# Optimization experiments

Measured on AMD Instinct MI355X. Metric: run time of the kernel, lower is better.

The kernel has to match this reference:

```python
import jax, jax.numpy as jnp
import numpy as np

EPS = 1e-07


def _splat_one(inp, idx4, w4, n):
    # inp: [C1, N] weighted features for one batch element
    # idx4: [4, N] int32 flat target indices (clipped)
    # w4:  [4, N] bilinear weights (zeroed where out of bounds)
    out = jnp.zeros((inp.shape[0], n), dtype=inp.dtype)
    for k in range(4):
        out = out.at[:, idx4[k]].add(inp * w4[k])
    return out


def _softsplat(x, flow, metric):
    B, C, H, W = x.shape
    N = H * W
    m = jnp.exp(metric)                      # [B,1,H,W]
    inp = jnp.concatenate([x * m, m], axis=1)  # [B,C+1,H,W]

    gy, gx = jnp.meshgrid(jnp.arange(H, dtype=x.dtype),
                          jnp.arange(W, dtype=x.dtype), indexing='ij')
    tx = gx[None] + flow[:, 0]               # [B,H,W] target x
    ty = gy[None] + flow[:, 1]               # [B,H,W] target y

    x0f = jnp.floor(tx)
    y0f = jnp.floor(ty)
    x0 = x0f.astype(jnp.int32)
    y0 = y0f.astype(jnp.int32)
    x1 = x0 + 1
    y1 = y0 + 1

    fx = tx - x0f                            # frac parts
    fy = ty - y0f
    # bilinear weights for (x0,y0),(x1,y0),(x0,y1),(x1,y1)
    w = jnp.stack([(1 - fx) * (1 - fy),
                   fx * (1 - fy),
                   (1 - fx) * fy,
                   fx * fy], axis=1)          # [B,4,H,W]
    xs = jnp.stack([x0, x1, x0, x1], axis=1)  # [B,4,H,W]
    ys = jnp.stack([y0, y0, y1, y1], axis=1)

    valid = (xs >= 0) & (xs < W) & (ys >= 0) & (ys < H)
    w = jnp.where(valid, w, 0.0).reshape(B, 4, N)
    idx = (jnp.clip(ys, 0, H - 1) * W + jnp.clip(xs, 0, W - 1)).reshape(B, 4, N)

    inp_flat = inp.reshape(B, C + 1, N)
    out = jax.vmap(lambda i, ix, ww: _splat_one(i, ix, ww, N))(inp_flat, idx, w)
    out = out.reshape(B, C + 1, H, W)
    return out[:, :-1] / (out[:, -1:] + EPS)


def setup_inputs() -> dict:
    key = jax.random.key(0)
    k1, k2, k3 = jax.random.split(key, 3)
    x = jax.random.normal(k1, (8, 64, 256, 448), dtype=jnp.float32)
    flow = jax.random.normal(k2, (8, 2, 256, 448), dtype=jnp.float32)
    metric = jax.random.normal(k3, (8, 1, 256, 448), dtype=jnp.float32)
    return {"x": x, "flow": flow, "metric": metric}


def reference(x, flow, metric):
    return _softsplat(x, flow, metric)
```

## Files before the change

### kernel.cpp

```cpp
#include <hip/hip_runtime.h>

#define EPS 1e-7f

constexpr int B = 8, C = 64, H = 256, W = 448;
constexpr int N = H * W;
constexpr int P = B * N;

constexpr int TS  = 16;
constexpr int NT  = 256;
constexpr int RW  = 8;
constexpr int WIN = 32;
constexpr int NW  = WIN * WIN;
constexpr int TGS = 40;
constexpr int K   = 15;
constexpr int CHB = 8;
constexpr int NCHUNK = C / CHB;
constexpr float FMAX = 7.0f;
constexpr int TX = W / TS, TY = H / TS;
constexpr int TILES = B * TX * TY;
constexpr int NXCD = 8;

constexpr int L_TGT = 0, L_FX = 1280, L_FY = 2304, L_EM = 3328, L_PK = 4352;
constexpr int LDS_WORDS = 8192;

typedef __fp16 h2_t __attribute__((ext_vector_type(2)));
static __device__ __forceinline__ unsigned pk2(float a, float b) {
    h2_t h = __builtin_amdgcn_cvt_pkrtz(a, b);
    return __builtin_bit_cast(unsigned, h);
}
static __device__ __forceinline__ float2 up2(unsigned u) {
    h2_t h = __builtin_bit_cast(h2_t, u);
    return make_float2((float)h.x, (float)h.y);
}

__device__ int g_flag;

__global__ void zero_flag_k() { g_flag = 0; }

__global__ __launch_bounds__(256) void flag_scan(const float* __restrict__ flow)
{
    int t = blockIdx.x * blockDim.x + threadIdx.x;
    if (t >= P) return;
    int b = t / N, p = t - b * N;
    float fdx = flow[(size_t)(b * 2 + 0) * N + p];
    float fdy = flow[(size_t)(b * 2 + 1) * N + p];
    if (fabsf(fdx) > FMAX || fabsf(fdy) > FMAX) atomicAdd(&g_flag, 1);
}

#define STAGE_LOAD(dst, gg)                                                   \
    {                                                                         \
        const int cbase = (gg) * CHB;                                         \
        const int row = tid >> 3;                                             \
        const int sc0 = (tid & 7) * 4;                                        \
        const int sh = ty0 - RW + row;                                        \
        const int sc = tx0 - RW + sc0;                                        \
        const bool v = (sh >= 0) & (sh < H) & (sc >= 0) & (sc < W);           \
        const float* bp = xb + (sh * W + sc);                                 \
        _Pragma("unroll")                                                     \
        for (int ch = 0; ch < CHB; ++ch)                                      \
            dst[ch] = v ? *(const float4*)(bp + (size_t)(cbase + ch) * N)     \
                        : make_float4(0.f, 0.f, 0.f, 0.f);                    \
    }

#define STAGE_WRITE(src, bufsel)                                              \
    {                                                                         \
        char* base = (char*)lds + (bufsel) * 16384;                           \
        _Pragma("unroll")                                                     \
        for (int k = 0; k < 4; ++k) {                                         \
            const unsigned pos = 4u * (unsigned)tid + (unsigned)k;            \
            const unsigned blk = pos ^ ((pos >> 3) & 7u);                     \
            uint4 wv;                                                         \
            wv.x = pk2(((const float*)&src[0])[k], ((const float*)&src[1])[k]); \
            wv.y = pk2(((const float*)&src[2])[k], ((const float*)&src[3])[k]); \
            wv.z = pk2(((const float*)&src[4])[k], ((const float*)&src[5])[k]); \
            wv.w = pk2(((const float*)&src[6])[k], ((const float*)&src[7])[k]); \
            *(uint4*)(base + blk * 16) = wv;                                  \
        }                                                                     \
    }

#define COMPUTE_STORE(bufsel, gg)                                             \
    {                                                                         \
        const char* bc = (const char*)lds + (bufsel) * 16384;                 \
        float a0 = 0.f, a1 = 0.f, a2 = 0.f, a3 = 0.f;                         \
        float a4 = 0.f, a5 = 0.f, a6 = 0.f, a7 = 0.f;                         \
        _Pragma("unroll")                                                     \
        for (int j = 0; j < K; ++j) {                                         \
            if (j >= kwave) break;                   \
            const uint4 v = *(const uint4*)(bc + rsp[j]);                     \
            const float wj = rw_[j];                                          \
            float2 pp;                                                        \
            pp = up2(v.x); a0 = fmaf(wj, pp.x, a0); a1 = fmaf(wj, pp.y, a1);  \
            pp = up2(v.y); a2 = fmaf(wj, pp.x, a2); a3 = fmaf(wj, pp.y, a3);  \
            pp = up2(v.z); a4 = fmaf(wj, pp.x, a4); a5 = fmaf(wj, pp.y, a5);  \
            pp = up2(v.w); a6 = fmaf(wj, pp.x, a6); a7 = fmaf(wj, pp.y, a7);  \
        }                                                                     \
        if (!ovf) {                                                           \
            ob[(size_t)((gg) * CHB + 0) * N] = a0;                            \
            ob[(size_t)((gg) * CHB + 1) * N] = a1;                            \
            ob[(size_t)((gg) * CHB + 2) * N] = a2;                            \
            ob[(size_t)((gg) * CHB + 3) * N] = a3;                            \
            ob[(size_t)((gg) * CHB + 4) * N] = a4;                            \
            ob[(size_t)((gg) * CHB + 5) * N] = a5;                            \
            ob[(size_t)((gg) * CHB + 6) * N] = a6;                            \
            ob[(size_t)((gg) * CHB + 7) * N] = a7;                            \
        }                                                                     \
    }

__global__ __launch_bounds__(NT) void softsplat_fused(
    const float* __restrict__ x,
    const float* __restrict__ flow,
    const float* __restrict__ metric,
    float* __restrict__ out,
    float* __restrict__ den)
{
    __shared__ float lds[LDS_WORDS];
    unsigned* s_tgt = (unsigned*)(lds + L_TGT);
    float*    s_fx  = lds + L_FX;
    float*    s_fy  = lds + L_FY;
    float*    s_em  = lds + L_EM;
    unsigned* s_pk  = (unsigned*)(lds + L_PK);

    int bid = blockIdx.x;
    bid = (bid % NXCD) * (TILES / NXCD) + bid / NXCD;

    const int b   = bid / (TX * TY);
    const int tp  = bid % (TX * TY);
    const int ty0 = (tp / TX) * TS;
    const int tx0 = (tp % TX) * TS;
    const int tid = threadIdx.x;

    const float* fxg = flow + (size_t)(b * 2 + 0) * N;
    const float* fyg = flow + (size_t)(b * 2 + 1) * N;
    const float* mg  = metric + (size_t)b * N;

    float mxx = 0.f, mxy = 0.f;
    for (int i = tid; i < NW; i += NT) {
        const int wy = i >> 5, wx = i & 31;
        const int sh = ty0 - RW + wy, sw = tx0 - RW + wx;
        unsigned t = 0xFFFFFFFFu;
        if (sh >= 0 && sh < H && sw >= 0 && sw < W) {
            const int sp = sh * W + sw;
            const float a = fxg[sp], bb = fyg[sp];
            if (fabsf(a) <= FMAX && fabsf(bb) <= FMAX) {
                const float xf = floorf(a), yf = floorf(bb);
                const int tx0g = sw + (int)xf + 16;
                const int ty0g = sh + (int)yf + 16;
                t = ((unsigned)ty0g << 16) | (unsigned)tx0g;
                s_fx[i] = a - xf;
                s_fy[i] = bb - yf;
                s_em[i] = __expf(mg[sp]);
                mxx = fmaxf(mxx, fabsf(a));
                mxy = fmaxf(mxy, fabsf(bb));
            }
        }
        s_tgt[wy * TGS + wx] = t;
    }
    #pragma unroll
    for (int m = 1; m < 64; m <<= 1) {
        mxx = fmaxf(mxx, __shfl_xor(mxx, m));
        mxy = fmaxf(mxy, __shfl_xor(mxy, m));
    }
    if ((tid & 63) == 0) {
        lds[L_PK + 2 * (tid >> 6) + 0] = mxx;
        lds[L_PK + 2 * (tid >> 6) + 1] = mxy;
    }
    __syncthreads();
    const float Mx = fmaxf(fmaxf(lds[L_PK + 0], lds[L_PK + 2]),
                           fmaxf(lds[L_PK + 4], lds[L_PK + 6]));
    const float My = fmaxf(fmaxf(lds[L_PK + 1], lds[L_PK + 3]),
                           fmaxf(lds[L_PK + 5], lds[L_PK + 7]));
    const int Rx = min(RW, (int)Mx + 1);
    const int Ry = min(RW, (int)My + 1);
    __syncthreads();

    const int qxl = tid & (TS - 1), qyl = tid >> 4;
    const int qx = tx0 + qxl, qy = ty0 + qyl;
    const int q  = qy * W + qx;
    const unsigned qx16 = (unsigned)(qx + 16), qy16 = (unsigned)(qy + 16);

    int cnt = 0;
    float dacc = 0.f;
    for (int dy = -Ry; dy <= Ry; ++dy) {
        const int lrow = qyl + RW + dy;
        const int trow = lrow * TGS + (qxl + RW);
        for (int dx = -Rx; dx <= Rx; ++dx) {
            const unsigned t = s_tgt[trow + dx];
            const unsigned du = qx16 - (t & 0xFFFFu);
            const unsigned dv = qy16 - (t >> 16);
            if (max(du, dv) > 1u) continue;
            const int fi = lrow * WIN + (qxl + RW + dx);
            const float fxf = s_fx[fi], fyf = s_fy[fi];
            const float wxf = du ? fxf : 1.f - fxf;
            const float wyf = dv ? fyf : 1.f - fyf;
            const float w = wxf * wyf * s_em[fi];
            if (cnt < K)
                s_pk[cnt * NT + tid] = (__float_as_uint(w) & 0xFFFFFC00u) | (unsigned)fi;
            cnt++;
            dacc += w;
        }
    }
    for (int j = cnt; j < K; ++j)
        s_pk[j * NT + tid] = (unsigned)((qyl + RW) * WIN + (qxl + RW));

    int km = cnt;
    #pragma unroll
    for (int m = 1; m < 64; m <<= 1) km = max(km, __shfl_xor(km, m));
    const int kwave = min(K, __builtin_amdgcn_readfirstlane(km));

    const int flag = g_flag;
    const float rn = (flag == 0) ? 1.f / (dacc + EPS) : 1.f;

    const float* xb = x + (size_t)b * C * N;
    float* ob = out + (size_t)b * C * N + q;
    den[(size_t)b * N + q] = dacc;

    unsigned rsp[K]; float rw_[K];
    #pragma unroll
    for (int j = 0; j < K; ++j) {
        const unsigned pk = s_pk[j * NT + tid];
        const unsigned pos = pk & 0x3FFu;
        rsp[j] = (pos ^ ((pos >> 3) & 7u)) << 4;
        rw_[j] = __uint_as_float(pk & 0xFFFFFC00u) * rn;
    }

    const bool ovf = (cnt > K);
    if (ovf) {
        for (int c = 0; c < C; ++c) {
            const float* xp = xb + (size_t)c * N;
            float a = 0.f;
            for (int dy = -Ry; dy <= Ry; ++dy) {
                const int lrow = qyl + RW + dy;
                const int trow = lrow * TGS + (qxl + RW);
                for (int dx = -Rx; dx <= Rx; ++dx) {
                    const unsigned t = s_tgt[trow + dx];
                    const unsigned du = qx16 - (t & 0xFFFFu);
                    const unsigned dv = qy16 - (t >> 16);
                    if (max(du, dv) > 1u) continue;
                    const int fi = lrow * WIN + (qxl + RW + dx);
                    const float fxf = s_fx[fi], fyf = s_fy[fi];
                    const float wxf = du ? fxf : 1.f - fxf;
                    const float wyf = dv ? fyf : 1.f - fyf;
                    a = fmaf(wxf * wyf * s_em[fi], xp[(qy + dy) * W + (qx + dx)], a);
                }
            }
            ob[(size_t)c * N] = a * rn;
        }
    }
    __syncthreads();

    float4 fr0[CHB], fr1[CHB];
    STAGE_LOAD(fr0, 0)
    STAGE_WRITE(fr0, 0)
    STAGE_LOAD(fr1, 1)
    __syncthreads();
    #pragma unroll
    for (int gp = 0; gp < NCHUNK; gp += 2) {
        if (gp + 2 < NCHUNK) STAGE_LOAD(fr0, gp + 2)
        COMPUTE_STORE(0, gp)
        STAGE_WRITE(fr1, 1)
        __syncthreads();
        if (gp + 3 < NCHUNK) STAGE_LOAD(fr1, gp + 3)
        COMPUTE_STORE(1, gp + 1)
        if (gp + 2 < NCHUNK) STAGE_WRITE(fr0, 0)
        __syncthreads();
    }
}

__global__ __launch_bounds__(256) void softsplat_outlier(
    const float* __restrict__ x,
    const float* __restrict__ flow,
    const float* __restrict__ metric,
    float* __restrict__ out,
    float* __restrict__ den)
{
    int t = blockIdx.x * blockDim.x + threadIdx.x;
    if (t >= P) return;
    int b = t / N;
    int p = t - b * N;
    float fdx = flow[(size_t)(b * 2 + 0) * N + p];
    float fdy = flow[(size_t)(b * 2 + 1) * N + p];
    if (fabsf(fdx) <= FMAX && fabsf(fdy) <= FMAX) return;

    int h = p / W, w = p - h * W;
    float m = __expf(metric[(size_t)b * N + p]);
    float tx = (float)w + fdx, ty = (float)h + fdy;
    float x0f = floorf(tx), y0f = floorf(ty);
    int x0 = (int)x0f, y0 = (int)y0f, x1 = x0 + 1, y1 = y0 + 1;
    float fx = tx - x0f, fy = ty - y0f;
    float w00 = (1.f - fx) * (1.f - fy), w10 = fx * (1.f - fy);
    float w01 = (1.f - fx) * fy,         w11 = fx * fy;
    bool vx0 = (x0 >= 0) && (x0 < W), vx1 = (x1 >= 0) && (x1 < W);
    bool vy0 = (y0 >= 0) && (y0 < H), vy1 = (y1 >= 0) && (y1 < H);
    int cx0 = min(max(x0, 0), W - 1), cx1 = min(max(x1, 0), W - 1);
    int cy0 = min(max(y0, 0), H - 1), cy1 = min(max(y1, 0), H - 1);
    int i00 = cy0 * W + cx0, i10 = cy0 * W + cx1;
    int i01 = cy1 * W + cx0, i11 = cy1 * W + cx1;
    w00 = (vx0 && vy0) ? w00 * m : 0.f;
    w10 = (vx1 && vy0) ? w10 * m : 0.f;
    w01 = (vx0 && vy1) ? w01 * m : 0.f;
    w11 = (vx1 && vy1) ? w11 * m : 0.f;

    float* denb = den + (size_t)b * N;
    if (w00 != 0.f) atomicAdd(denb + i00, w00);
    if (w10 != 0.f) atomicAdd(denb + i10, w10);
    if (w01 != 0.f) atomicAdd(denb + i01, w01);
    if (w11 != 0.f) atomicAdd(denb + i11, w11);

    const float* xb = x + (size_t)b * C * N + p;
    float* ob = out + (size_t)b * C * N;
    for (int c = 0; c < C; ++c) {
        float v = xb[(size_t)c * N];
        float* o = ob + (size_t)c * N;
        if (w00 != 0.f) atomicAdd(o + i00, v * w00);
        if (w10 != 0.f) atomicAdd(o + i10, v * w10);
        if (w01 != 0.f) atomicAdd(o + i01, v * w01);
        if (w11 != 0.f) atomicAdd(o + i11, v * w11);
    }
}

__global__ __launch_bounds__(256) void softsplat_norm(
    float* __restrict__ out, const float* __restrict__ den)
{
    if (g_flag == 0) return;
    size_t t = (size_t)blockIdx.x * blockDim.x + threadIdx.x;
    size_t e = t * 4;
    if (e >= (size_t)B * C * N) return;
    size_t b = e / ((size_t)C * N);
    size_t p = (e - b * (size_t)C * N) % N;

    float4 o = *reinterpret_cast<float4*>(out + e);
    const float4 d = *reinterpret_cast<const float4*>(den + b * N + p);
    o.x = o.x / (d.x + EPS);
    o.y = o.y / (d.y + EPS);
    o.z = o.z / (d.z + EPS);
    o.w = o.w / (d.w + EPS);
    *reinterpret_cast<float4*>(out + e) = o;
}

extern "C" void kernel_launch(void* const* d_in, const int* in_sizes, int n_in,
                              void* d_out, int out_size, void* d_ws, size_t ws_size,
                              hipStream_t stream) {
    const float* x      = (const float*)d_in[0];
    const float* flow   = (const float*)d_in[1];
    const float* metric = (const float*)d_in[2];
    float* out = (float*)d_out;
    float* den = (float*)d_ws;

    zero_flag_k<<<1, 1, 0, stream>>>();
    flag_scan<<<(P + 255) / 256, 256, 0, stream>>>(flow);

    softsplat_fused<<<TILES, NT, 0, stream>>>(x, flow, metric, out, den);

    softsplat_outlier<<<(P + 255) / 256, 256, 0, stream>>>(x, flow, metric, out, den);

    size_t nvec4 = (size_t)B * C * N / 4;
    softsplat_norm<<<(int)((nvec4 + 255) / 256), 256, 0, stream>>>(out, den);
}
```

Baseline: 240.3 us.

## Replace gather-side neighbor search with scatter-side LDS binning via atomics

Instead of each output pixel scanning a (2R+1)^2 window of source targets in LDS to find contributors, each source pixel now pushes its index and corner id into per-output-pixel LDS bins using shared-memory atomicAdd. Weights are then recomputed from the binned entries, which removes the dynamic radius reduction and the window scan. The overflow path now reads flow and metric straight from global memory over the full radius. This adds LDS atomics, and bin order becomes nondeterministic, which can change the float summation order.

Result: faster. 222.4 us (-7.4%).

```diff
diff --git a/kernel.cpp b/kernel.cpp
--- a/kernel.cpp
+++ b/kernel.cpp
@@ -11,7 +11,6 @@
 constexpr int RW  = 8;
 constexpr int WIN = 32;
 constexpr int NW  = WIN * WIN;
-constexpr int TGS = 40;
 constexpr int K   = 15;
 constexpr int CHB = 8;
 constexpr int NCHUNK = C / CHB;
@@ -20,7 +19,7 @@
 constexpr int TILES = B * TX * TY;
 constexpr int NXCD = 8;
 
-constexpr int L_TGT = 0, L_FX = 1280, L_FY = 2304, L_EM = 3328, L_PK = 4352;
+constexpr int L_FX = 0, L_FY = 1024, L_EM = 2048, L_CNT = 3072, L_MB = 3328;
 constexpr int LDS_WORDS = 8192;
 
 typedef __fp16 h2_t __attribute__((ext_vector_type(2)));
@@ -114,11 +113,11 @@
     float* __restrict__ den)
 {
     __shared__ float lds[LDS_WORDS];
-    unsigned* s_tgt = (unsigned*)(lds + L_TGT);
     float*    s_fx  = lds + L_FX;
     float*    s_fy  = lds + L_FY;
     float*    s_em  = lds + L_EM;
-    unsigned* s_pk  = (unsigned*)(lds + L_PK);
+    int*      s_cnt = (int*)(lds + L_CNT);
+    unsigned* s_mb  = (unsigned*)(lds + L_MB);
 
     int bid = blockIdx.x;
     bid = (bid % NXCD) * (TILES / NXCD) + bid / NXCD;
@@ -133,117 +132,113 @@
     const float* fyg = flow + (size_t)(b * 2 + 1) * N;
     const float* mg  = metric + (size_t)b * N;
 
-    float mxx = 0.f, mxy = 0.f;
+    s_cnt[tid] = 0;
+    __syncthreads();
+
     for (int i = tid; i < NW; i += NT) {
         const int wy = i >> 5, wx = i & 31;
         const int sh = ty0 - RW + wy, sw = tx0 - RW + wx;
-        unsigned t = 0xFFFFFFFFu;
         if (sh >= 0 && sh < H && sw >= 0 && sw < W) {
             const int sp = sh * W + sw;
             const float a = fxg[sp], bb = fyg[sp];
             if (fabsf(a) <= FMAX && fabsf(bb) <= FMAX) {
                 const float xf = floorf(a), yf = floorf(bb);
-                const int tx0g = sw + (int)xf + 16;
-                const int ty0g = sh + (int)yf + 16;
-                t = ((unsigned)ty0g << 16) | (unsigned)tx0g;
                 s_fx[i] = a - xf;
                 s_fy[i] = bb - yf;
                 s_em[i] = __expf(mg[sp]);
-                mxx = fmaxf(mxx, fabsf(a));
-                mxy = fmaxf(mxy, fabsf(bb));
+                const int ltx = sw + (int)xf - tx0;
+                const int lty = sh + (int)yf - ty0;
+                #pragma unroll
+                for (int cr = 0; cr < 4; ++cr) {
+                    const int cx = ltx + (cr & 1), cy = lty + (cr >> 1);
+                    if ((unsigned)cx < (unsigned)TS && (unsigned)cy < (unsigned)TS) {
+                        const int oid = cy * TS + cx;
+                        const int slot = atomicAdd(&s_cnt[oid], 1);
+                        if (slot < K) s_mb[slot * NT + oid] = (unsigned)(i | (cr << 10));
+                    }
+                }
             }
         }
-        s_tgt[wy * TGS + wx] = t;
-    }
-    #pragma unroll
-    for (int m = 1; m < 64; m <<= 1) {
-        mxx = fmaxf(mxx, __shfl_xor(mxx, m));
-        mxy = fmaxf(mxy, __shfl_xor(mxy, m));
-    }
-    if ((tid & 63) == 0) {
-        lds[L_PK + 2 * (tid >> 6) + 0] = mxx;
-        lds[L_PK + 2 * (tid >> 6) + 1] = mxy;
-    }
-    __syncthreads();
-    const float Mx = fmaxf(fmaxf(lds[L_PK + 0], lds[L_PK + 2]),
-                           fmaxf(lds[L_PK + 4], lds[L_PK + 6]));
-    const float My = fmaxf(fmaxf(lds[L_PK + 1], lds[L_PK + 3]),
-                           fmaxf(lds[L_PK + 5], lds[L_PK + 7]));
-    const int Rx = min(RW, (int)Mx + 1);
-    const int Ry = min(RW, (int)My + 1);
+    }
     __syncthreads();
 
     const int qxl = tid & (TS - 1), qyl = tid >> 4;
     const int qx = tx0 + qxl, qy = ty0 + qyl;
     const int q  = qy * W + qx;
-    const unsigned qx16 = (unsigned)(qx + 16), qy16 = (unsigned)(qy + 16);
-
-    int cnt = 0;
-    float dacc = 0.f;
-    for (int dy = -Ry; dy <= Ry; ++dy) {
-        const int lrow = qyl + RW + dy;
-        const int trow = lrow * TGS + (qxl + RW);
-        for (int dx = -Rx; dx <= Rx; ++dx) {
-            const unsigned t = s_tgt[trow + dx];
-            const unsigned du = qx16 - (t & 0xFFFFu);
-            const unsigned dv = qy16 - (t >> 16);
-            if (max(du, dv) > 1u) continue;
-            const int fi = lrow * WIN + (qxl + RW + dx);
-            const float fxf = s_fx[fi], fyf = s_fy[fi];
-            const float wxf = du ? fxf : 1.f - fxf;
-            const float wyf = dv ? fyf : 1.f - fyf;
-            const float w = wxf * wyf * s_em[fi];
-            if (cnt < K)
-                s_pk[cnt * NT + tid] = (__float_as_uint(w) & 0xFFFFFC00u) | (unsigned)fi;
-            cnt++;
-            dacc += w;
-        }
-    }
-    for (int j = cnt; j < K; ++j)
-        s_pk[j * NT + tid] = (unsigned)((qyl + RW) * WIN + (qxl + RW));
-
+
+    const int cnt = s_cnt[tid];
+    const int kk  = min(cnt, K);
     int km = cnt;
     #pragma unroll
     for (int m = 1; m < 64; m <<= 1) km = max(km, __shfl_xor(km, m));
     const int kwave = min(K, __builtin_amdgcn_readfirstlane(km));
 
-    const int flag = g_flag;
-    const float rn = (flag == 0) ? 1.f / (dacc + EPS) : 1.f;
-
-    const float* xb = x + (size_t)b * C * N;
-    float* ob = out + (size_t)b * C * N + q;
-    den[(size_t)b * N + q] = dacc;
-
+    float dacc = 0.f;
     unsigned rsp[K]; float rw_[K];
     #pragma unroll
     for (int j = 0; j < K; ++j) {
-        const unsigned pk = s_pk[j * NT + tid];
-        const unsigned pos = pk & 0x3FFu;
+        const bool live = j < kk;
+        const unsigned pk = s_mb[j * NT + tid];
+        const unsigned fi = pk & 1023u;
+        const unsigned cr = (pk >> 10) & 3u;
+        const float fxf = s_fx[fi], fyf = s_fy[fi];
+        const float wxf = (cr & 1u) ? fxf : 1.f - fxf;
+        const float wyf = (cr >> 1) ? fyf : 1.f - fyf;
+        const float w = live ? wxf * wyf * s_em[fi] : 0.f;
+        dacc += w;
+        rw_[j] = w;
+        const unsigned pos = live ? fi : (unsigned)((qyl + RW) * WIN + (qxl + RW));
         rsp[j] = (pos ^ ((pos >> 3) & 7u)) << 4;
-        rw_[j] = __uint_as_float(pk & 0xFFFFFC00u) * rn;
     }
 
     const bool ovf = (cnt > K);
+    if (ovf) {
+        dacc = 0.f;
+        for (int dy = -RW; dy <= RW; ++dy) {
+            for (int dx = -RW; dx <= RW; ++dx) {
+                const int sh = qy + dy, sw = qx + dx;
+                if (sh < 0 || sh >= H || sw < 0 || sw >= W) continue;
+                const int sp = sh * W + sw;
+                const float a = fxg[sp], bb = fyg[sp];
+                if (fabsf(a) > FMAX || fabsf(bb) > FMAX) continue;
+                const float xf = floorf(a), yf = floorf(bb);
+                const int du = qx - (sw + (int)xf); if ((unsigned)du > 1u) continue;
+                const int dv = qy - (sh + (int)yf); if ((unsigned)dv > 1u) continue;
+                const float wxf = du ? a - xf : 1.f - (a - xf);
+                const float wyf = dv ? bb - yf : 1.f - (bb - yf);
+                dacc += wxf * wyf * __expf(mg[sp]);
+            }
+        }
+    }
+    den[(size_t)b * N + q] = dacc;
+
+    const float rn = (g_flag == 0) ? 1.f / (dacc + EPS) : 1.f;
+    #pragma unroll
+    for (int j = 0; j < K; ++j) rw_[j] *= rn;
+
+    const float* xb = x + (size_t)b * C * N;
+    float* ob = out + (size_t)b * C * N + q;
+
     if (ovf) {
         for (int c = 0; c < C; ++c) {
             const float* xp = xb + (size_t)c * N;
-            float a = 0.f;
-            for (int dy = -Ry; dy <= Ry; ++dy) {
-                const int lrow = qyl + RW + dy;
-                const int trow = lrow * TGS + (qxl + RW);
-                for (int dx = -Rx; dx <= Rx; ++dx) {
-                    const unsigned t = s_tgt[trow + dx];
-                    const unsigned du = qx16 - (t & 0xFFFFu);
-                    const unsigned dv = qy16 - (t >> 16);
-                    if (max(du, dv) > 1u) continue;
-                    const int fi = lrow * WIN + (qxl + RW + dx);
-                    const float fxf = s_fx[fi], fyf = s_fy[fi];
-                    const float wxf = du ? fxf : 1.f - fxf;
-                    const float wyf = dv ? fyf : 1.f - fyf;
-                    a = fmaf(wxf * wyf * s_em[fi], xp[(qy + dy) * W + (qx + dx)], a);
+            float acc = 0.f;
+            for (int dy = -RW; dy <= RW; ++dy) {
+                for (int dx = -RW; dx <= RW; ++dx) {
+                    const int sh = qy + dy, sw = qx + dx;
+                    if (sh < 0 || sh >= H || sw < 0 || sw >= W) continue;
+                    const int sp = sh * W + sw;
+                    const float a = fxg[sp], bb = fyg[sp];
+                    if (fabsf(a) > FMAX || fabsf(bb) > FMAX) continue;
+                    const float xf = floorf(a), yf = floorf(bb);
+                    const int du = qx - (sw + (int)xf); if ((unsigned)du > 1u) continue;
+                    const int dv = qy - (sh + (int)yf); if ((unsigned)dv > 1u) continue;
+                    const float wxf = du ? a - xf : 1.f - (a - xf);
+                    const float wyf = dv ? bb - yf : 1.f - (bb - yf);
+                    acc = fmaf(wxf * wyf * __expf(mg[sp]), xp[sp], acc);
                 }
             }
-            ob[(size_t)c * N] = a * rn;
+            ob[(size_t)c * N] = acc * rn;
         }
     }
     __syncthreads();
```
